# Kernel tuning notes

Measured on AMD Instinct MI355X. Metric: run time of the kernel, lower is better.

## Reference

```python
import jax, jax.numpy as jnp
import numpy as np

L, MODS, D, R, B, T = 2, 3, 512, 32, 16, 512  # nlayers, n_modals, embed_dim, rank, batch, length
BETA = 0.1


def setup_inputs() -> dict:
    key = jax.random.key(0)
    ks = jax.random.split(key, 12)
    s_in = 1.0 / np.sqrt(D)      # nn.Linear default init scale for d->R projections
    s_att = 1.0 / np.sqrt(R * R)  # for (R*R)->d projection

    def w(k, shape, scale):
        return jax.random.uniform(k, shape, jnp.float32, -scale, scale)

    return {
        "x_a": jax.random.normal(ks[0], (B, T, D), jnp.float32),
        "x_t": jax.random.normal(ks[1], (B, T, D), jnp.float32),
        "x_v": jax.random.normal(ks[2], (B, T, D), jnp.float32),
        # stacked per-layer, per-modality params
        "Wq1": w(ks[3], (L, MODS, D, R), s_in), "bq1": w(ks[4], (L, MODS, R), s_in),
        "Wq2": w(ks[5], (L, MODS, D, R), s_in), "bq2": w(ks[6], (L, MODS, R), s_in),
        "Wk1": w(ks[7], (L, MODS, D, R), s_in), "bk1": w(ks[8], (L, MODS, R), s_in),
        "Wk2": w(ks[9], (L, MODS, D, R), s_in), "bk2": w(ks[10], (L, MODS, R), s_in),
        "Watt": w(ks[11], (L, MODS, R * R, D), s_att),
        "batt": jnp.zeros((L, MODS, D), jnp.float32),
    }


def _proj(X, W, b):
    # X: [M,B,T,D], W: [M,D,R], b: [M,R] -> [M,B,T,R]
    return jnp.einsum('mbtd,mdr->mbtr', X, W) + b[:, None, None, :]


def reference(x_a, x_t, x_v, Wq1, bq1, Wq2, bq2, Wk1, bk1, Wk2, bk2, Watt, batt):
    X = jnp.stack([x_a, x_t, x_v])  # [M,B,T,D]
    for li in range(L):
        q1 = _proj(X, Wq1[li], bq1[li])
        q2 = _proj(X, Wq2[li], bq2[li])
        k1 = _proj(X, Wk1[li], bk1[li])
        k2 = _proj(X, Wk2[li], bk2[li])
        # low-rank bilinear maps: G_qk[j] = (q1 outer q2) * (k1 outer k2) -> [M,B,T,R,R]
        G = (q1[..., :, None] * q2[..., None, :]) * (k1[..., :, None] * k2[..., None, :])
        Mqk = G.mean(axis=2)  # [M,B,R,R] mean over time
        outs = []
        for j in range(MODS):
            # chained cross-modal contraction == G_j @ (prod_{l!=j, ascending} M_l)
            P = None
            for l in range(MODS):
                if l == j:
                    continue
                P = Mqk[l] if P is None else jnp.einsum('bkl,blo->bko', P, Mqk[l])
            att = jnp.einsum('btkl,blo->btko', G[j], P)  # [B,T,R,R]
            flat = att.reshape(B, T, R * R)
            proj = flat @ Watt[li, j] + batt[li, j]  # [B,T,D]
            outs.append(proj * X[j] + BETA * X[j])  # residual combine (dropout is eval-mode identity)
        X = jnp.stack(outs)
    return X[0], X[1], X[2]
```

## Files before the change

### kernel.cpp

```cpp
#include <hip/hip_runtime.h>

#define L_ 2
#define MODS_ 3
#define D_ 512
#define R_ 32
#define B_ 16
#define T_ 512
#define BT_ (B_*T_)
#define BETA_ 0.1f

typedef _Float16 h8 __attribute__((ext_vector_type(8)));
typedef __fp16   fp16x2 __attribute__((ext_vector_type(2)));
typedef float f32x16 __attribute__((ext_vector_type(16)));

typedef __attribute__((address_space(3))) unsigned int lds_u32;
typedef __attribute__((address_space(1))) const unsigned int glb_u32;

__device__ __forceinline__ void gload_lds16(const uint4* gsrc, uint4* ldst){
    __builtin_amdgcn_global_load_lds((glb_u32*)gsrc, (lds_u32*)ldst, 16, 0, 0);
}

#define WAITVM(N) asm volatile("s_waitcnt vmcnt(" #N ")" ::: "memory")
#define SBAR() __builtin_amdgcn_s_barrier()

__device__ __forceinline__ h8 mk_h8(float f0,float f1,float f2,float f3,
                                    float f4,float f5,float f6,float f7){
    union { h8 v; fp16x2 p[4]; } r;
    r.p[0] = __builtin_amdgcn_cvt_pkrtz(f0,f1);
    r.p[1] = __builtin_amdgcn_cvt_pkrtz(f2,f3);
    r.p[2] = __builtin_amdgcn_cvt_pkrtz(f4,f5);
    r.p[3] = __builtin_amdgcn_cvt_pkrtz(f6,f7);
    return r.v;
}
__device__ __forceinline__ float h2f(unsigned short x){
    return (float)__builtin_bit_cast(_Float16, x);
}
__device__ __forceinline__ unsigned short f2h(float x){
    return __builtin_bit_cast(unsigned short, (_Float16)x);
}

__global__ __launch_bounds__(256) void k_cvt(
    const float* __restrict__ Watt,
    const float* __restrict__ Wq1, const float* __restrict__ Wk1,
    const float* __restrict__ Wq2, const float* __restrict__ Wk2,
    uint4* __restrict__ WattF, uint4* __restrict__ WprojF)
{
    const int t = blockIdx.x*256 + threadIdx.x;
    const int NWATT = 6*32*16*2*64;
    if (t < NWATT) {
        const int lane = t & 63, f = t >> 6;
        const int kh = f & 1, nb = (f>>1)&15, s = (f>>5)&31, lj = f>>10;
        const int col  = nb*32 + (lane&31);
        const int row0 = s*32 + kh*16 + (lane>>5)*8;
        const float* src = Watt + ((size_t)lj*1024)*D_ + col;
        union { uint4 q; unsigned short us[8]; } o;
        #pragma unroll
        for (int i=0;i<8;i++) o.us[i] = f2h(src[(size_t)(row0+i)*D_]);
        WattF[t] = o.q;
    } else {
        const int t2 = t - NWATT;
        const int lane = t2 & 63, f = t2 >> 6;
        const int nb = f & 3, s = (f>>2)&31, lm = f>>7;
        const float* Ws = (nb==0)?Wq1:(nb==1)?Wk1:(nb==2)?Wq2:Wk2;
        const int r  = lane&31;
        const int k0 = s*16 + (lane>>5)*8;
        const float* src = Ws + ((size_t)lm*D_)*R_ + r;
        union { uint4 q; unsigned short us[8]; } o;
        #pragma unroll
        for (int i=0;i<8;i++) o.us[i] = f2h(src[(size_t)(k0+i)*R_]);
        WprojF[t2] = o.q;
    }
}

__global__ __launch_bounds__(256) void k_proj_mfma(
    const float* __restrict__ xa, const float* __restrict__ xt,
    const float* __restrict__ xv, const float* __restrict__ X,
    const uint4* __restrict__ WprojF,
    const float* __restrict__ bq1, const float* __restrict__ bq2,
    const float* __restrict__ bk1, const float* __restrict__ bk2,
    unsigned short* __restrict__ U16, unsigned short* __restrict__ V16, int li)
{
    __shared__ uint4 sm[4][512];
    const int tid = threadIdx.x;
    const int wid = tid>>6, lane = tid&63;
    const int lh = lane>>5, lr = lane&31;
    const int wtok = wid&1, pair = wid>>1;
    const int m = blockIdx.y;
    const int tok0 = blockIdx.x*64;
    const int lm = li*MODS_ + m;
    const int t = tok0 + wtok*32 + lr;

    const float* Xbase = (li==0) ? (m==0?xa:(m==1?xt:xv)) : (X + (size_t)m*BT_*D_);
    const float* Xrow  = Xbase + (size_t)t*D_;
    const uint4* srcp  = WprojF + (size_t)lm*8192;

    f32x16 accQ, accK;
    #pragma unroll
    for (int i=0;i<16;i++){ accQ[i]=0.f; accK[i]=0.f; }

    float4 xr[2][2][2];

#define PJ_XLOAD(T) do{ \
        xr[(T)&1][0][0] = *(const float4*)&Xrow[(T)*32      + lh*8]; \
        xr[(T)&1][0][1] = *(const float4*)&Xrow[(T)*32      + lh*8 + 4]; \
        xr[(T)&1][1][0] = *(const float4*)&Xrow[(T)*32 + 16 + lh*8]; \
        xr[(T)&1][1][1] = *(const float4*)&Xrow[(T)*32 + 16 + lh*8 + 4]; \
    }while(0)

#define PJ_STAGE(S,BUF) do{ \
        gload_lds16(srcp + (S)*512       + tid, &sm[BUF][wid*64]); \
        gload_lds16(srcp + (S)*512 + 256 + tid, &sm[BUF][256 + wid*64]); \
    }while(0)

#define PJ_COMP(T) do{ \
        const uint4 bq0_ = sm[(T)&3][        (pair*2  )*64 + lane]; \
        const uint4 bk0_ = sm[(T)&3][        (pair*2+1)*64 + lane]; \
        const uint4 bq1_ = sm[(T)&3][256 +   (pair*2  )*64 + lane]; \
        const uint4 bk1_ = sm[(T)&3][256 +   (pair*2+1)*64 + lane]; \
        const float4 xlo0 = xr[(T)&1][0][0], xhi0 = xr[(T)&1][0][1]; \
        const float4 xlo1 = xr[(T)&1][1][0], xhi1 = xr[(T)&1][1][1]; \
        h8 a0 = mk_h8(xlo0.x,xlo0.y,xlo0.z,xlo0.w, xhi0.x,xhi0.y,xhi0.z,xhi0.w); \
        h8 a1 = mk_h8(xlo1.x,xlo1.y,xlo1.z,xlo1.w, xhi1.x,xhi1.y,xhi1.z,xhi1.w); \
        accQ = __builtin_amdgcn_mfma_f32_32x32x16_f16(a0, __builtin_bit_cast(h8,bq0_), accQ, 0,0,0); \
        accK = __builtin_amdgcn_mfma_f32_32x32x16_f16(a0, __builtin_bit_cast(h8,bk0_), accK, 0,0,0); \
        accQ = __builtin_amdgcn_mfma_f32_32x32x16_f16(a1, __builtin_bit_cast(h8,bq1_), accQ, 0,0,0); \
        accK = __builtin_amdgcn_mfma_f32_32x32x16_f16(a1, __builtin_bit_cast(h8,bk1_), accK, 0,0,0); \
    }while(0)

    PJ_XLOAD(0);
    PJ_STAGE(0,0); PJ_STAGE(1,1); PJ_STAGE(2,2);

    WAITVM(4); SBAR();
    PJ_XLOAD(1); PJ_STAGE(3,3); PJ_COMP(0);

    #pragma unroll
    for (int tt=1; tt<=12; ++tt){
        WAITVM(8); SBAR();
        PJ_XLOAD(tt+1);
        PJ_STAGE(tt+3, (tt+3)&3);
        PJ_COMP(tt);
    }
    WAITVM(8); SBAR(); PJ_XLOAD(14); PJ_COMP(13);
    WAITVM(6); SBAR(); PJ_XLOAD(15); PJ_COMP(14);
    WAITVM(4); SBAR(); PJ_COMP(15);

    const float bA = (pair==0 ? bq1 : bq2)[lm*R_ + lr];
    const float bB = (pair==0 ? bk1 : bk2)[lm*R_ + lr];
    unsigned short* Out = (pair==0 ? U16 : V16);
    #pragma unroll
    for (int reg=0;reg<16;reg++){
        const int row = (reg&3) + 8*(reg>>2) + 4*lh;
        const int tt  = tok0 + wtok*32 + row;
        const float val = (accQ[reg]+bA)*(accK[reg]+bB)*64.f;
        Out[((size_t)m*BT_ + tt)*R_ + lr] = f2h(val);
    }
#undef PJ_XLOAD
#undef PJ_STAGE
#undef PJ_COMP
}

__global__ __launch_bounds__(256) void k_mqk_part(
    const unsigned short* __restrict__ U16,
    const unsigned short* __restrict__ V16,
    float* __restrict__ Mqp)
{
    const int tid = threadIdx.x;
    const int mb  = blockIdx.x;
    const int p   = blockIdx.y;
    const int t0  = p*64;

    __shared__ unsigned short Us[64][32];
    __shared__ unsigned short Vs[64][32];

    const int srow = tid>>2, sq = (tid&3)*8;
    const size_t base = (size_t)mb*T_*R_ + (size_t)(t0+srow)*R_ + sq;
    *(uint4*)&Us[srow][sq] = *(const uint4*)&U16[base];
    *(uint4*)&Vs[srow][sq] = *(const uint4*)&V16[base];
    __syncthreads();

    const int l = tid & 31;
    const int g = tid >> 5;
    float acc[4] = {0.f,0.f,0.f,0.f};
    #pragma unroll 8
    for (int tt=0; tt<64; ++tt){
        const float vv = h2f(Vs[tt][l]);
        #pragma unroll
        for (int i=0;i<4;i++) acc[i] += h2f(Us[tt][g+8*i]) * vv;
    }
    float* out = Mqp + ((size_t)p*48 + mb)*1024;
    #pragma unroll
    for (int i=0;i<4;i++) out[(g+8*i)*R_ + l] = acc[i];
}

__global__ __launch_bounds__(256) void k_wvec_fused(
    const float* __restrict__ Mqp,
    const unsigned short* __restrict__ V16,
    unsigned short* __restrict__ W16)
{
    const int tid  = threadIdx.x;
    const int j    = blockIdx.y;
    const int tok0 = blockIdx.x * 128;
    const int b    = tok0 / T_;
    const int a = (j==0) ? 1 : 0;
    const int c = (j==2) ? 1 : 2;
    const float sc = 1.0f/(4096.0f*(float)T_);

    __shared__ float As[32][32];
    __shared__ float Cs[32][32];
    __shared__ float Ps[32][32];
    __shared__ unsigned short Vs[128][32];

    float4 sa = {0,0,0,0}, sc4 = {0,0,0,0};
    #pragma unroll
    for (int p=0;p<8;p++){
        const float4 pa = *(const float4*)&Mqp[((size_t)p*48 + a*B_+b)*1024 + tid*4];
        const float4 pc = *(const float4*)&Mqp[((size_t)p*48 + c*B_+b)*1024 + tid*4];
        sa.x+=pa.x; sa.y+=pa.y; sa.z+=pa.z; sa.w+=pa.w;
        sc4.x+=pc.x; sc4.y+=pc.y; sc4.z+=pc.z; sc4.w+=pc.w;
    }
    sa.x*=sc; sa.y*=sc; sa.z*=sc; sa.w*=sc;
    sc4.x*=sc; sc4.y*=sc; sc4.z*=sc; sc4.w*=sc;
    *(float4*)&(((float*)As)[tid*4]) = sa;
    *(float4*)&(((float*)Cs)[tid*4]) = sc4;

    const unsigned short* Vb = V16 + ((size_t)j*BT_ + tok0)*R_;
    #pragma unroll
    for (int e=0;e<2;e++){
        const int k = tid*2 + e;
        *(uint4*)&Vs[k>>2][(k&3)*8] = *(const uint4*)&Vb[(size_t)(k>>2)*R_ + (k&3)*8];
    }
    __syncthreads();

    const int o = tid & 31, g = tid >> 5;
    {
        float acc[4] = {0.f,0.f,0.f,0.f};
        #pragma unroll
        for (int l = 0; l < 32; ++l) {
            const float cvv = Cs[l][o];
            #pragma unroll
            for (int i = 0; i < 4; ++i) acc[i] += As[g + 8*i][l] * cvv;
        }
        #pragma unroll
        for (int i = 0; i < 4; ++i) Ps[g + 8*i][o] = acc[i];
    }
    __syncthreads();

    unsigned short* Wb = W16 + ((size_t)j*BT_ + tok0)*R_;
    #pragma unroll
    for (int i = 0; i < 16; ++i) {
        const int t = g*16 + i;
        float acc = 0.f;
        #pragma unroll
        for (int l = 0; l < 32; ++l) acc += h2f(Vs[t][l]) * Ps[l][o];
        Wb[(size_t)t*R_ + o] = f2h(acc);
    }
}

__global__ __launch_bounds__(256) void k_gemm2_mfma(
    const unsigned short* __restrict__ U16,
    const unsigned short* __restrict__ W16,
    const uint4* __restrict__ WattF, const float* __restrict__ batt,
    const float* __restrict__ xa, const float* __restrict__ xt,
    const float* __restrict__ xv,
    float* __restrict__ X, int li)
{
    __shared__ uint4 sm[4][256];
    const int tid = threadIdx.x;
    const int wid = tid>>6, lane = tid&63;
    const int lh = lane>>5, lr = lane&31;
    const int wtok = wid&1, wcol = wid>>1;
    const int j = blockIdx.z;
    const int tok0 = blockIdx.x*128;
    const int t0 = tok0 + wtok*64 + lr;
    const int t1 = t0 + 32;

    const uint4* src = WattF + (size_t)(li*MODS_ + j)*65536 + (size_t)blockIdx.y*256;

    union { uint4 q[4]; __fp16 h[32]; } uu0, uu1;
    {
        const uint4* Ur0 = (const uint4*)(U16 + ((size_t)j*BT_ + t0)*R_);
        const uint4* Ur1 = (const uint4*)(U16 + ((size_t)j*BT_ + t1)*R_);
        uu0.q[0]=Ur0[0]; uu0.q[1]=Ur0[1]; uu0.q[2]=Ur0[2]; uu0.q[3]=Ur0[3];
        uu1.q[0]=Ur1[0]; uu1.q[1]=Ur1[1]; uu1.q[2]=Ur1[2]; uu1.q[3]=Ur1[3];
    }
    union { uint4 q; fp16x2 p[4]; } wa0, wb0, wa1, wb1;
    {
        const uint4* Wr0 = (const uint4*)(W16 + ((size_t)j*BT_ + t0)*R_);
        const uint4* Wr1 = (const uint4*)(W16 + ((size_t)j*BT_ + t1)*R_);
        wa0.q = Wr0[lh]; wb0.q = Wr0[2+lh];
        wa1.q = Wr1[lh]; wb1.q = Wr1[2+lh];
    }

    f32x16 acc0, acc1;
    #pragma unroll
    for (int i=0;i<16;i++){ acc0[i]=0.f; acc1[i]=0.f; }

#define G2_STAGE(S,BUF) gload_lds16(src + (S)*2048 + tid, &sm[BUF][wid*64])

#define G2_COMP(T) do{ \
        const uint4 b0_ = sm[(T)&3][(wcol*2  )*64 + lane]; \
        const uint4 b1_ = sm[(T)&3][(wcol*2+1)*64 + lane]; \
        fp16x2 u0s, u1s; u0s[0]=uu0.h[T]; u0s[1]=uu0.h[T]; u1s[0]=uu1.h[T]; u1s[1]=uu1.h[T]; \
        union { h8 v; fp16x2 p[4]; } a00,a01,a10,a11; \
        _Pragma("unroll") \
        for (int q_=0;q_<4;q_++){ \
            a00.p[q_]=u0s*wa0.p[q_]; a01.p[q_]=u0s*wb0.p[q_]; \
            a10.p[q_]=u1s*wa1.p[q_]; a11.p[q_]=u1s*wb1.p[q_]; \
        } \
        acc0 = __builtin_amdgcn_mfma_f32_32x32x16_f16(a00.v, __builtin_bit_cast(h8,b0_), acc0, 0,0,0); \
        acc1 = __builtin_amdgcn_mfma_f32_32x32x16_f16(a10.v, __builtin_bit_cast(h8,b0_), acc1, 0,0,0); \
        acc0 = __builtin_amdgcn_mfma_f32_32x32x16_f16(a01.v, __builtin_bit_cast(h8,b1_), acc0, 0,0,0); \
        acc1 = __builtin_amdgcn_mfma_f32_32x32x16_f16(a11.v, __builtin_bit_cast(h8,b1_), acc1, 0,0,0); \
    }while(0)

    G2_STAGE(0,0); G2_STAGE(1,1); G2_STAGE(2,2);

    #pragma unroll
    for (int tt=0; tt<30; ++tt){
        WAITVM(2); SBAR();
        if (tt < 29) G2_STAGE(tt+3, (tt+3)&3);
        G2_COMP(tt);
    }
    WAITVM(1); SBAR(); G2_COMP(30);
    WAITVM(0); SBAR(); G2_COMP(31);

    const float* battp = batt + (size_t)(li*MODS_ + j)*D_;
    const float* Xin = (li==0) ? (j==0?xa:(j==1?xt:xv)) : (X + (size_t)j*BT_*D_);
    float* Xout = X + (size_t)j*BT_*D_;
    const float inv = 1.0f/4096.0f;
    const int d = blockIdx.y*64 + wcol*32 + lr;
    const float bt = battp[d];
    #pragma unroll
    for (int reg=0; reg<16; ++reg){
        const int row = (reg&3) + 8*(reg>>2) + 4*lh;
        const size_t xi0 = (size_t)(tok0 + wtok*64 + row)*D_ + d;
        const size_t xi1 = (size_t)(tok0 + wtok*64 + 32 + row)*D_ + d;
        const float xv0 = Xin[xi0], xv1 = Xin[xi1];
        Xout[xi0] = (acc0[reg]*inv + bt)*xv0 + BETA_*xv0;
        Xout[xi1] = (acc1[reg]*inv + bt)*xv1 + BETA_*xv1;
    }
#undef G2_STAGE
#undef G2_COMP
}

extern "C" void kernel_launch(void* const* d_in, const int* in_sizes, int n_in,
                              void* d_out, int out_size, void* d_ws, size_t ws_size,
                              hipStream_t stream)
{
    const float* x_a  = (const float*)d_in[0];
    const float* x_t  = (const float*)d_in[1];
    const float* x_v  = (const float*)d_in[2];
    const float* Wq1  = (const float*)d_in[3];
    const float* bq1  = (const float*)d_in[4];
    const float* Wq2  = (const float*)d_in[5];
    const float* bq2  = (const float*)d_in[6];
    const float* Wk1  = (const float*)d_in[7];
    const float* bk1  = (const float*)d_in[8];
    const float* Wk2  = (const float*)d_in[9];
    const float* bk2  = (const float*)d_in[10];
    const float* Watt = (const float*)d_in[11];
    const float* batt = (const float*)d_in[12];

    float* X = (float*)d_out;

    uint4* WattF  = (uint4*)d_ws;
    uint4* WprojF = WattF + 393216;
    float* Mqp    = (float*)(WprojF + 49152);
    unsigned short* U16 = (unsigned short*)(Mqp + 393216);
    unsigned short* V16 = U16 + (size_t)MODS_*BT_*R_;
    unsigned short* W16 = V16 + (size_t)MODS_*BT_*R_;

    k_cvt<<<1728, 256, 0, stream>>>(Watt, Wq1, Wk1, Wq2, Wk2, WattF, WprojF);

    for (int li = 0; li < L_; ++li) {
        k_proj_mfma<<<dim3(BT_/64, MODS_), 256, 0, stream>>>(
            x_a, x_t, x_v, X, WprojF, bq1, bq2, bk1, bk2, U16, V16, li);
        k_mqk_part<<<dim3(MODS_*B_, 8), 256, 0, stream>>>(U16, V16, Mqp);
        k_wvec_fused<<<dim3(BT_/128, MODS_), 256, 0, stream>>>(Mqp, V16, W16);
        k_gemm2_mfma<<<dim3(BT_/128, D_/64, MODS_), 256, 0, stream>>>(
            U16, W16, WattF, batt, x_a, x_t, x_v, X, li);
    }
}
```

Before: 287.6 us.

## Widen gemm2 output tile to 128 columns and deepen prefetch pipelines

The attention-projection GEMM now computes 128 output columns per block instead of 64, with each wave holding four accumulators. This halves the grid along D and reuses the per-token A fragments (built from U and W) across twice as many columns, so the elementwise fp16 products and the U/W reads are done half as often. Its LDS staging grows to a 6-deep ring of larger tiles. The projection kernel also prefetches X rows two steps ahead instead of one. The changes raise register and LDS use and leave fewer blocks in flight.

Result: slower. 308.1 us (+7.1%).

```diff
diff --git a/kernel.cpp b/kernel.cpp
--- a/kernel.cpp
+++ b/kernel.cpp
@@ -98,13 +98,13 @@
     #pragma unroll
     for (int i=0;i<16;i++){ accQ[i]=0.f; accK[i]=0.f; }
 
-    float4 xr[2][2][2];
+    float4 xr[3][2][2];
 
 #define PJ_XLOAD(T) do{ \
-        xr[(T)&1][0][0] = *(const float4*)&Xrow[(T)*32      + lh*8]; \
-        xr[(T)&1][0][1] = *(const float4*)&Xrow[(T)*32      + lh*8 + 4]; \
-        xr[(T)&1][1][0] = *(const float4*)&Xrow[(T)*32 + 16 + lh*8]; \
-        xr[(T)&1][1][1] = *(const float4*)&Xrow[(T)*32 + 16 + lh*8 + 4]; \
+        xr[(T)%3][0][0] = *(const float4*)&Xrow[(T)*32      + lh*8]; \
+        xr[(T)%3][0][1] = *(const float4*)&Xrow[(T)*32      + lh*8 + 4]; \
+        xr[(T)%3][1][0] = *(const float4*)&Xrow[(T)*32 + 16 + lh*8]; \
+        xr[(T)%3][1][1] = *(const float4*)&Xrow[(T)*32 + 16 + lh*8 + 4]; \
     }while(0)
 
 #define PJ_STAGE(S,BUF) do{ \
@@ -117,8 +117,8 @@
         const uint4 bk0_ = sm[(T)&3][        (pair*2+1)*64 + lane]; \
         const uint4 bq1_ = sm[(T)&3][256 +   (pair*2  )*64 + lane]; \
         const uint4 bk1_ = sm[(T)&3][256 +   (pair*2+1)*64 + lane]; \
-        const float4 xlo0 = xr[(T)&1][0][0], xhi0 = xr[(T)&1][0][1]; \
-        const float4 xlo1 = xr[(T)&1][1][0], xhi1 = xr[(T)&1][1][1]; \
+        const float4 xlo0 = xr[(T)%3][0][0], xhi0 = xr[(T)%3][0][1]; \
+        const float4 xlo1 = xr[(T)%3][1][0], xhi1 = xr[(T)%3][1][1]; \
         h8 a0 = mk_h8(xlo0.x,xlo0.y,xlo0.z,xlo0.w, xhi0.x,xhi0.y,xhi0.z,xhi0.w); \
         h8 a1 = mk_h8(xlo1.x,xlo1.y,xlo1.z,xlo1.w, xhi1.x,xhi1.y,xhi1.z,xhi1.w); \
         accQ = __builtin_amdgcn_mfma_f32_32x32x16_f16(a0, __builtin_bit_cast(h8,bq0_), accQ, 0,0,0); \
@@ -127,22 +127,21 @@
         accK = __builtin_amdgcn_mfma_f32_32x32x16_f16(a1, __builtin_bit_cast(h8,bk1_), accK, 0,0,0); \
     }while(0)
 
-    PJ_XLOAD(0);
+    PJ_XLOAD(0); PJ_XLOAD(1);
     PJ_STAGE(0,0); PJ_STAGE(1,1); PJ_STAGE(2,2);
 
     WAITVM(4); SBAR();
-    PJ_XLOAD(1); PJ_STAGE(3,3); PJ_COMP(0);
-
-    #pragma unroll
-    for (int tt=1; tt<=12; ++tt){
+    PJ_XLOAD(2); PJ_STAGE(3,3); PJ_COMP(0);
+
+    #pragma unroll
+    for (int tt=1; tt<=13; ++tt){
         WAITVM(8); SBAR();
-        PJ_XLOAD(tt+1);
-        PJ_STAGE(tt+3, (tt+3)&3);
+        PJ_XLOAD(tt+2);
+        if (tt <= 12) PJ_STAGE(tt+3, (tt+3)&3);
         PJ_COMP(tt);
     }
-    WAITVM(8); SBAR(); PJ_XLOAD(14); PJ_COMP(13);
-    WAITVM(6); SBAR(); PJ_XLOAD(15); PJ_COMP(14);
-    WAITVM(4); SBAR(); PJ_COMP(15);
+    WAITVM(6); SBAR(); PJ_COMP(14);
+    WAITVM(0); SBAR(); PJ_COMP(15);
 
     const float bA = (pair==0 ? bq1 : bq2)[lm*R_ + lr];
     const float bB = (pair==0 ? bk1 : bk2)[lm*R_ + lr];
@@ -264,7 +263,7 @@
     const float* __restrict__ xv,
     float* __restrict__ X, int li)
 {
-    __shared__ uint4 sm[4][256];
+    __shared__ uint4 sm[6][512];
     const int tid = threadIdx.x;
     const int wid = tid>>6, lane = tid&63;
     const int lh = lane>>5, lr = lane&31;
@@ -274,7 +273,7 @@
     const int t0 = tok0 + wtok*64 + lr;
     const int t1 = t0 + 32;
 
-    const uint4* src = WattF + (size_t)(li*MODS_ + j)*65536 + (size_t)blockIdx.y*256;
+    const uint4* src = WattF + (size_t)(li*MODS_ + j)*65536 + (size_t)blockIdx.y*512;
 
     union { uint4 q[4]; __fp16 h[32]; } uu0, uu1;
     {
@@ -291,15 +290,21 @@
         wa1.q = Wr1[lh]; wb1.q = Wr1[2+lh];
     }
 
-    f32x16 acc0, acc1;
-    #pragma unroll
-    for (int i=0;i<16;i++){ acc0[i]=0.f; acc1[i]=0.f; }
-
-#define G2_STAGE(S,BUF) gload_lds16(src + (S)*2048 + tid, &sm[BUF][wid*64])
+    f32x16 acc00, acc01, acc10, acc11;
+    #pragma unroll
+    for (int i=0;i<16;i++){ acc00[i]=0.f; acc01[i]=0.f; acc10[i]=0.f; acc11[i]=0.f; }
+
+#define G2_STAGE(S,BUF) do{ \
+        gload_lds16(src + (size_t)(S)*2048       + tid, &sm[BUF][      wid*64]); \
+        gload_lds16(src + (size_t)(S)*2048 + 256 + tid, &sm[BUF][256 + wid*64]); \
+    }while(0)
 
 #define G2_COMP(T) do{ \
-        const uint4 b0_ = sm[(T)&3][(wcol*2  )*64 + lane]; \
-        const uint4 b1_ = sm[(T)&3][(wcol*2+1)*64 + lane]; \
+        const int nb0_ = wcol*2, nb1_ = wcol*2+1; \
+        const uint4 b00_ = sm[(T)%6][(nb0_*2  )*64 + lane]; \
+        const uint4 b01_ = sm[(T)%6][(nb0_*2+1)*64 + lane]; \
+        const uint4 b10_ = sm[(T)%6][(nb1_*2  )*64 + lane]; \
+        const uint4 b11_ = sm[(T)%6][(nb1_*2+1)*64 + lane]; \
         fp16x2 u0s, u1s; u0s[0]=uu0.h[T]; u0s[1]=uu0.h[T]; u1s[0]=uu1.h[T]; u1s[1]=uu1.h[T]; \
         union { h8 v; fp16x2 p[4]; } a00,a01,a10,a11; \
         _Pragma("unroll") \
@@ -307,37 +312,49 @@
             a00.p[q_]=u0s*wa0.p[q_]; a01.p[q_]=u0s*wb0.p[q_]; \
             a10.p[q_]=u1s*wa1.p[q_]; a11.p[q_]=u1s*wb1.p[q_]; \
         } \
-        acc0 = __builtin_amdgcn_mfma_f32_32x32x16_f16(a00.v, __builtin_bit_cast(h8,b0_), acc0, 0,0,0); \
-        acc1 = __builtin_amdgcn_mfma_f32_32x32x16_f16(a10.v, __builtin_bit_cast(h8,b0_), acc1, 0,0,0); \
-        acc0 = __builtin_amdgcn_mfma_f32_32x32x16_f16(a01.v, __builtin_bit_cast(h8,b1_), acc0, 0,0,0); \
-        acc1 = __builtin_amdgcn_mfma_f32_32x32x16_f16(a11.v, __builtin_bit_cast(h8,b1_), acc1, 0,0,0); \
+        acc00 = __builtin_amdgcn_mfma_f32_32x32x16_f16(a00.v, __builtin_bit_cast(h8,b00_), acc00, 0,0,0); \
+        acc10 = __builtin_amdgcn_mfma_f32_32x32x16_f16(a10.v, __builtin_bit_cast(h8,b00_), acc10, 0,0,0); \
+        acc01 = __builtin_amdgcn_mfma_f32_32x32x16_f16(a00.v, __builtin_bit_cast(h8,b10_), acc01, 0,0,0); \
+        acc11 = __builtin_amdgcn_mfma_f32_32x32x16_f16(a10.v, __builtin_bit_cast(h8,b10_), acc11, 0,0,0); \
+        acc00 = __builtin_amdgcn_mfma_f32_32x32x16_f16(a01.v, __builtin_bit_cast(h8,b01_), acc00, 0,0,0); \
+        acc10 = __builtin_amdgcn_mfma_f32_32x32x16_f16(a11.v, __builtin_bit_cast(h8,b01_), acc10, 0,0,0); \
+        acc01 = __builtin_amdgcn_mfma_f32_32x32x16_f16(a01.v, __builtin_bit_cast(h8,b11_), acc01, 0,0,0); \
+        acc11 = __builtin_amdgcn_mfma_f32_32x32x16_f16(a11.v, __builtin_bit_cast(h8,b11_), acc11, 0,0,0); \
     }while(0)
 
-    G2_STAGE(0,0); G2_STAGE(1,1); G2_STAGE(2,2);
-
-    #pragma unroll
-    for (int tt=0; tt<30; ++tt){
-        WAITVM(2); SBAR();
-        if (tt < 29) G2_STAGE(tt+3, (tt+3)&3);
+    G2_STAGE(0,0); G2_STAGE(1,1); G2_STAGE(2,2); G2_STAGE(3,3); G2_STAGE(4,4);
+
+    #pragma unroll
+    for (int tt=0; tt<28; ++tt){
+        WAITVM(8); SBAR();
+        if (tt < 27) G2_STAGE(tt+5, (tt+5)%6);
         G2_COMP(tt);
     }
-    WAITVM(1); SBAR(); G2_COMP(30);
+    WAITVM(6); SBAR(); G2_COMP(28);
+    WAITVM(4); SBAR(); G2_COMP(29);
+    WAITVM(2); SBAR(); G2_COMP(30);
     WAITVM(0); SBAR(); G2_COMP(31);
 
     const float* battp = batt + (size_t)(li*MODS_ + j)*D_;
     const float* Xin = (li==0) ? (j==0?xa:(j==1?xt:xv)) : (X + (size_t)j*BT_*D_);
     float* Xout = X + (size_t)j*BT_*D_;
     const float inv = 1.0f/4096.0f;
-    const int d = blockIdx.y*64 + wcol*32 + lr;
-    const float bt = battp[d];
-    #pragma unroll
-    for (int reg=0; reg<16; ++reg){
-        const int row = (reg&3) + 8*(reg>>2) + 4*lh;
-        const size_t xi0 = (size_t)(tok0 + wtok*64 + row)*D_ + d;
-        const size_t xi1 = (size_t)(tok0 + wtok*64 + 32 + row)*D_ + d;
-        const float xv0 = Xin[xi0], xv1 = Xin[xi1];
-        Xout[xi0] = (acc0[reg]*inv + bt)*xv0 + BETA_*xv0;
-        Xout[xi1] = (acc1[reg]*inv + bt)*xv1 + BETA_*xv1;
+    const int dbase = blockIdx.y*128 + wcol*64 + lr;
+    #pragma unroll
+    for (int ni=0; ni<2; ++ni){
+        const int d = dbase + ni*32;
+        const float bt = battp[d];
+        const f32x16& aL = ni ? acc01 : acc00;
+        const f32x16& aH = ni ? acc11 : acc10;
+        #pragma unroll
+        for (int reg=0; reg<16; ++reg){
+            const int row = (reg&3) + 8*(reg>>2) + 4*lh;
+            const size_t xi0 = (size_t)(tok0 + wtok*64 + row)*D_ + d;
+            const size_t xi1 = (size_t)(tok0 + wtok*64 + 32 + row)*D_ + d;
+            const float xv0 = Xin[xi0], xv1 = Xin[xi1];
+            Xout[xi0] = (aL[reg]*inv + bt)*xv0 + BETA_*xv0;
+            Xout[xi1] = (aH[reg]*inv + bt)*xv1 + BETA_*xv1;
+        }
     }
 #undef G2_STAGE
 #undef G2_COMP
@@ -377,7 +394,7 @@
             x_a, x_t, x_v, X, WprojF, bq1, bq2, bk1, bk2, U16, V16, li);
         k_mqk_part<<<dim3(MODS_*B_, 8), 256, 0, stream>>>(U16, V16, Mqp);
         k_wvec_fused<<<dim3(BT_/128, MODS_), 256, 0, stream>>>(Mqp, V16, W16);
-        k_gemm2_mfma<<<dim3(BT_/128, D_/64, MODS_), 256, 0, stream>>>(
+        k_gemm2_mfma<<<dim3(BT_/128, D_/128, MODS_), 256, 0, stream>>>(
             U16, W16, WattF, batt, x_a, x_t, x_v, X, li);
     }
 }
```
